# Performance work log

Hardware: AMD Instinct MI355X
Metric: run time of the kernel (lower is better)

## Reference

```python
import jax, jax.numpy as jnp
import numpy as np

VTHR = 1.0


def setup_inputs() -> dict:
    key = jax.random.key(0)
    k1, k2, k3 = jax.random.split(key, 3)
    B, T, IN, OUT = 256, 8, 4096, 4096
    x = jax.random.normal(k1, (B * T, IN), dtype=jnp.float32)
    weight_scaled = jax.random.normal(k2, (OUT, IN), dtype=jnp.float32) * 0.02
    bias_scaled = jax.random.normal(k3, (OUT,), dtype=jnp.float32) * 0.02
    return {"x": x, "weight_scaled": weight_scaled, "bias_scaled": bias_scaled, "timesteps": T}


def _spike_linear(x, weight_scaled, bias_scaled, timesteps):
    # F.linear: [B*T, IN] @ [OUT, IN]^T + [OUT]
    out = jnp.dot(x, weight_scaled.T) + bias_scaled  # [B*T, OUT]
    OUT = out.shape[-1]
    out_s = out.reshape(-1, timesteps, OUT)  # [B, T, OUT]
    out_t = jnp.transpose(out_s, (1, 0, 2))  # [T, B, OUT] for scan

    def step(memb, o_t):
        memb = memb + VTHR * o_t
        spike = (memb > VTHR).astype(out.dtype)
        memb = memb * (1.0 - spike)  # reset_mode == 'zero'
        return memb, spike

    memb0 = jnp.zeros(out_t.shape[1:], dtype=out.dtype)
    _, spikes = jax.lax.scan(step, memb0, out_t)  # [T, B, OUT]
    # torch.cat(spikes, 0): t-major concat -> [T*B, OUT]
    return spikes.reshape(-1, OUT)


def reference(x, weight_scaled, bias_scaled, timesteps):
    return _spike_linear(x, weight_scaled, bias_scaled, timesteps)
```

## Files before the change

### kernel.cpp

```cpp
#include <hip/hip_runtime.h>


typedef float v2f __attribute__((ext_vector_type(2)));

#define PK_LO(a, x, wv)                                                       \
    asm("v_pk_fma_f32 %0, %1, %2, %0 op_sel:[0,0,0] op_sel_hi:[0,1,1]"        \
        : "+v"(a) : "v"(x), "v"(wv))
#define PK_HI(a, x, wv)                                                       \
    asm("v_pk_fma_f32 %0, %1, %2, %0 op_sel:[1,0,0] op_sel_hi:[1,1,1]"        \
        : "+v"(a) : "v"(x), "v"(wv))

constexpr int TSTEPS = 8;
constexpr int BK     = 16;
constexpr int TILE_M = 64;
constexpr int TILE_NP= 256;
constexpr int TILE_N = 128;
constexpr int KC     = 384;

__global__ __launch_bounds__(256, 2)
void spike_panel_gemm(const float* __restrict__ x,
                      const float* __restrict__ w,
                      float* __restrict__ panels,
                      float* __restrict__ out,
                      int slice0, int NW,
                      int B, int IN, int OUT, int npanels)
{
    __shared__ float xs[BK][TILE_M + 4];
    __shared__ float wsh[BK][TILE_NP + 8];

    const int tid  = threadIdx.x;
    const int lane = tid & 63;
    const int wv   = tid >> 6;
    const int rg   = lane >> 3;
    const int cg   = lane & 7;
    const int cbase = wv * 64 + cg * 8;

    const int m0 = blockIdx.y * TILE_M;
    const int n0 = slice0 + blockIdx.x * TILE_NP;
    const int p  = blockIdx.z;
    const int ks = p * KC;
    const int ke = (ks + KC < IN) ? (ks + KC) : IN;

    v2f acc[TSTEPS][4];
    #pragma unroll
    for (int t = 0; t < TSTEPS; ++t)
        #pragma unroll
        for (int q = 0; q < 4; ++q) acc[t][q] = (v2f){0.f, 0.f};

    const int sr = tid >> 2;
    const int sk = (tid & 3) * 4;

    const float* xrow  = x + (size_t)(m0 + sr) * IN + sk;
    const float* wrow0 = w + (size_t)(n0 +       sr) * IN + sk;
    const float* wrow1 = w + (size_t)(n0 +  64 + sr) * IN + sk;
    const float* wrow2 = w + (size_t)(n0 + 128 + sr) * IN + sk;
    const float* wrow3 = w + (size_t)(n0 + 192 + sr) * IN + sk;

    for (int kk = ks; kk < ke; kk += BK) {
        const float4 xv  = *(const float4*)(xrow  + kk);
        const float4 wv0 = *(const float4*)(wrow0 + kk);
        const float4 wv1 = *(const float4*)(wrow1 + kk);
        const float4 wv2 = *(const float4*)(wrow2 + kk);
        const float4 wv3 = *(const float4*)(wrow3 + kk);
        __syncthreads();
        xs[sk+0][sr] = xv.x;  xs[sk+1][sr] = xv.y;
        xs[sk+2][sr] = xv.z;  xs[sk+3][sr] = xv.w;
        wsh[sk+0][sr]     = wv0.x; wsh[sk+1][sr]     = wv0.y;
        wsh[sk+2][sr]     = wv0.z; wsh[sk+3][sr]     = wv0.w;
        wsh[sk+0][sr+64]  = wv1.x; wsh[sk+1][sr+64]  = wv1.y;
        wsh[sk+2][sr+64]  = wv1.z; wsh[sk+3][sr+64]  = wv1.w;
        wsh[sk+0][sr+128] = wv2.x; wsh[sk+1][sr+128] = wv2.y;
        wsh[sk+2][sr+128] = wv2.z; wsh[sk+3][sr+128] = wv2.w;
        wsh[sk+0][sr+192] = wv3.x; wsh[sk+1][sr+192] = wv3.y;
        wsh[sk+2][sr+192] = wv3.z; wsh[sk+3][sr+192] = wv3.w;
        __syncthreads();

        #pragma unroll
        for (int k = 0; k < BK; ++k) {
            v2f xp[4], wva[4];
            *(float4*)&xp[0]  = *(const float4*)&xs[k][rg*8];
            *(float4*)&xp[2]  = *(const float4*)&xs[k][rg*8 + 4];
            *(float4*)&wva[0] = *(const float4*)&wsh[k][cbase];
            *(float4*)&wva[2] = *(const float4*)&wsh[k][cbase + 4];
            #pragma unroll
            for (int tp = 0; tp < 4; ++tp) {
                #pragma unroll
                for (int q = 0; q < 4; ++q) {
                    PK_LO(acc[2*tp  ][q], xp[tp], wva[q]);
                    PK_HI(acc[2*tp+1][q], xp[tp], wva[q]);
                }
            }
        }
    }

    const int bg = blockIdx.y * 8 + rg;
    const int cs = blockIdx.x * TILE_NP + cbase;
    if (p < npanels - 1) {
        float* pb = panels + ((size_t)p * B * TSTEPS) * NW;
        #pragma unroll
        for (int t = 0; t < TSTEPS; ++t) {
            const int m = bg * TSTEPS + t;
            float4 lo, hi;
            *(v2f*)&lo.x = acc[t][0]; *(v2f*)&lo.z = acc[t][1];
            *(v2f*)&hi.x = acc[t][2]; *(v2f*)&hi.z = acc[t][3];
            *(float4*)(pb + (size_t)m * NW + cs)     = lo;
            *(float4*)(pb + (size_t)m * NW + cs + 4) = hi;
        }
    } else {
        const int o0 = n0 + cbase;
        #pragma unroll
        for (int t = 0; t < TSTEPS; ++t) {
            float4 lo, hi;
            *(v2f*)&lo.x = acc[t][0]; *(v2f*)&lo.z = acc[t][1];
            *(v2f*)&hi.x = acc[t][2]; *(v2f*)&hi.z = acc[t][3];
            float* op = out + ((size_t)t * B + bg) * OUT + o0;
            *(float4*)op       = lo;
            *(float4*)(op + 4) = hi;
        }
    }
}

__global__ __launch_bounds__(256)
void spike_fold_scan(const float* __restrict__ panels,
                     const float* __restrict__ bias,
                     float* __restrict__ out,
                     int slice0, int NW,
                     int B, int OUT, int npanels)
{
    const int b = blockIdx.y;
    const size_t psz = (size_t)B * TSTEPS * NW;
    const int nc4 = NW / 4;

    for (int c4 = blockIdx.x * 256 + threadIdx.x; c4 < nc4;
         c4 += gridDim.x * 256) {
        const int cs   = c4 * 4;
        const int gcol = slice0 + cs;

        float4 v[TSTEPS];
        #pragma unroll
        for (int t = 0; t < TSTEPS; ++t)
            v[t] = *(const float4*)(panels + (size_t)(b*TSTEPS + t) * NW + cs);
        for (int p = 1; p < npanels - 1; ++p) {
            const float* pb = panels + (size_t)p * psz;
            #pragma unroll
            for (int t = 0; t < TSTEPS; ++t) {
                const float4 u = *(const float4*)(pb + (size_t)(b*TSTEPS + t) * NW + cs);
                v[t].x += u.x; v[t].y += u.y; v[t].z += u.z; v[t].w += u.w;
            }
        }
        #pragma unroll
        for (int t = 0; t < TSTEPS; ++t) {
            const float4 u = *(const float4*)(out + ((size_t)t * B + b) * OUT + gcol);
            v[t].x += u.x; v[t].y += u.y; v[t].z += u.z; v[t].w += u.w;
        }

        const float4 bb = *(const float4*)(bias + gcol);
        float memb[4] = {0.f, 0.f, 0.f, 0.f};
        #pragma unroll
        for (int t = 0; t < TSTEPS; ++t) {
            float pre[4] = {v[t].x + bb.x, v[t].y + bb.y,
                            v[t].z + bb.z, v[t].w + bb.w};
            float4 sp;
            float* spp = (float*)&sp;
            #pragma unroll
            for (int c = 0; c < 4; ++c) {
                memb[c] += pre[c];
                float s = (memb[c] > 1.0f) ? 1.0f : 0.0f;
                memb[c] *= (1.0f - s);
                spp[c] = s;
            }
            *(float4*)(out + ((size_t)t * B + b) * OUT + gcol) = sp;
        }
    }
}

__global__ __launch_bounds__(256, 4)
void spike_linear_f32seq(const float* __restrict__ x,
                         const float* __restrict__ w,
                         const float* __restrict__ bias,
                         float* __restrict__ out,
                         int B, int IN, int OUT)
{
    __shared__ float xs[BK][TILE_M + 4];
    __shared__ float ws[BK][TILE_N + 4];

    const int tid = threadIdx.x;
    const int tx  = tid & 31;
    const int ty  = tid >> 5;

    const int m0 = blockIdx.y * TILE_M;
    const int n0 = blockIdx.x * TILE_N;

    float acc_tot[TSTEPS][4];
    float acc_blk[TSTEPS][4];
    #pragma unroll
    for (int t = 0; t < TSTEPS; ++t)
        #pragma unroll
        for (int c = 0; c < 4; ++c) { acc_tot[t][c] = 0.f; acc_blk[t][c] = 0.f; }

    const int sr = tid >> 2;
    const int sk = (tid & 3) * 4;

    const float* xrow  = x + (size_t)(m0 + sr) * IN + sk;
    const float* wrow0 = w + (size_t)(n0 + sr) * IN + sk;
    const float* wrow1 = w + (size_t)(n0 + 64 + sr) * IN + sk;

    for (int kk = 0; kk < IN; kk += BK) {
        if (kk > 0 && (kk % KC) == 0) {
            #pragma unroll
            for (int t = 0; t < TSTEPS; ++t)
                #pragma unroll
                for (int c = 0; c < 4; ++c) {
                    acc_tot[t][c] += acc_blk[t][c];
                    acc_blk[t][c] = 0.f;
                }
        }
        const float4 xv  = *(const float4*)(xrow  + kk);
        const float4 wv0 = *(const float4*)(wrow0 + kk);
        const float4 wv1 = *(const float4*)(wrow1 + kk);
        __syncthreads();
        xs[sk+0][sr] = xv.x;  xs[sk+1][sr] = xv.y;
        xs[sk+2][sr] = xv.z;  xs[sk+3][sr] = xv.w;
        ws[sk+0][sr]    = wv0.x; ws[sk+1][sr]    = wv0.y;
        ws[sk+2][sr]    = wv0.z; ws[sk+3][sr]    = wv0.w;
        ws[sk+0][sr+64] = wv1.x; ws[sk+1][sr+64] = wv1.y;
        ws[sk+2][sr+64] = wv1.z; ws[sk+3][sr+64] = wv1.w;
        __syncthreads();

        #pragma unroll
        for (int k = 0; k < BK; ++k) {
            float xr[TSTEPS];
            *(float4*)&xr[0] = *(const float4*)&xs[k][ty*8];
            *(float4*)&xr[4] = *(const float4*)&xs[k][ty*8 + 4];
            float wr[4];
            *(float4*)&wr[0] = *(const float4*)&ws[k][tx*4];
            #pragma unroll
            for (int t = 0; t < TSTEPS; ++t)
                #pragma unroll
                for (int c = 0; c < 4; ++c)
                    acc_blk[t][c] = fmaf(xr[t], wr[c], acc_blk[t][c]);
        }
    }
    #pragma unroll
    for (int t = 0; t < TSTEPS; ++t)
        #pragma unroll
        for (int c = 0; c < 4; ++c)
            acc_tot[t][c] += acc_blk[t][c];

    const int bg = blockIdx.y * 8 + ty;
    const int o0 = n0 + tx * 4;
    const float4 bv = *(const float4*)(bias + o0);
    const float bb[4] = {bv.x, bv.y, bv.z, bv.w};
    float memb[4] = {0.f, 0.f, 0.f, 0.f};
    #pragma unroll
    for (int t = 0; t < TSTEPS; ++t) {
        float4 sp;
        float* spp = (float*)&sp;
        #pragma unroll
        for (int c = 0; c < 4; ++c) {
            float pre = acc_tot[t][c] + bb[c];
            memb[c] += pre;
            float s = (memb[c] > 1.0f) ? 1.0f : 0.0f;
            memb[c] *= (1.0f - s);
            spp[c] = s;
        }
        *(float4*)(out + ((size_t)t * B + bg) * OUT + o0) = sp;
    }
}

extern "C" void kernel_launch(void* const* d_in, const int* in_sizes, int n_in,
                              void* d_out, int out_size, void* d_ws, size_t ws_size,
                              hipStream_t stream)
{
    const float* x    = (const float*)d_in[0];
    const float* w    = (const float*)d_in[1];
    const float* bias = (const float*)d_in[2];
    float* out = (float*)d_out;

    const int OUT = in_sizes[2];
    const int IN  = in_sizes[1] / OUT;
    const int BT  = in_sizes[0] / IN;
    const int B   = BT / TSTEPS;

    const int npanels = (IN + KC - 1) / KC;

    int NW = 0;
    for (int cand = 4096; cand >= 256; cand >>= 1) {
        if ((OUT % cand) == 0 &&
            (size_t)(npanels - 1) * BT * cand * sizeof(float) <= ws_size) {
            NW = cand;
            break;
        }
    }

    if (NW >= 256 && npanels >= 2) {
        float* panels = (float*)d_ws;
        const int nslices = OUT / NW;
        for (int s = 0; s < nslices; ++s) {
            const int slice0 = s * NW;
            dim3 g1(NW / TILE_NP, BT / TILE_M, npanels);
            spike_panel_gemm<<<g1, 256, 0, stream>>>(x, w, panels, out,
                                                     slice0, NW, B, IN, OUT,
                                                     npanels);
            int gx = NW / 1024; if (gx < 1) gx = 1;
            dim3 g2(gx, B);
            spike_fold_scan<<<g2, 256, 0, stream>>>(panels, bias, out,
                                                    slice0, NW, B, OUT,
                                                    npanels);
        }
    } else {
        dim3 grid(OUT / TILE_N, BT / TILE_M);
        spike_linear_f32seq<<<grid, 256, 0, stream>>>(x, w, bias, out, B, IN, OUT);
    }
}
```

Before: 827.3 us.

## Prefetch next K-tile into registers and split column groups to cut LDS conflicts

The GEMM main loop now issues the global loads for the next BK slice right after the LDS stores, so their latency overlaps the FMA work on the current slice (register double-buffering). Each lane's eight output columns are also split into two groups of four spaced 32 apart, with the shared-memory padding reduced accordingly, to change the LDS read pattern and reduce bank conflicts. Output stores follow the new column mapping. Keeping the prefetched tile in registers raises register pressure under launch_bounds(256,2), and K must be a multiple of BK.

```diff
diff --git a/kernel.cpp b/kernel.cpp
--- a/kernel.cpp
+++ b/kernel.cpp
@@ -16,6 +16,7 @@
 constexpr int TILE_NP= 256;
 constexpr int TILE_N = 128;
 constexpr int KC     = 384;
+constexpr int WS_PAD = 4;
 
 __global__ __launch_bounds__(256, 2)
 void spike_panel_gemm(const float* __restrict__ x,
@@ -26,14 +27,14 @@
                       int B, int IN, int OUT, int npanels)
 {
     __shared__ float xs[BK][TILE_M + 4];
-    __shared__ float wsh[BK][TILE_NP + 8];
+    __shared__ float wsh[BK][TILE_NP + WS_PAD];
 
     const int tid  = threadIdx.x;
     const int lane = tid & 63;
     const int wv   = tid >> 6;
     const int rg   = lane >> 3;
     const int cg   = lane & 7;
-    const int cbase = wv * 64 + cg * 8;
+    const int clo  = wv * 64 + cg * 4;
 
     const int m0 = blockIdx.y * TILE_M;
     const int n0 = slice0 + blockIdx.x * TILE_NP;
@@ -56,12 +57,15 @@
     const float* wrow2 = w + (size_t)(n0 + 128 + sr) * IN + sk;
     const float* wrow3 = w + (size_t)(n0 + 192 + sr) * IN + sk;
 
-    for (int kk = ks; kk < ke; kk += BK) {
-        const float4 xv  = *(const float4*)(xrow  + kk);
-        const float4 wv0 = *(const float4*)(wrow0 + kk);
-        const float4 wv1 = *(const float4*)(wrow1 + kk);
-        const float4 wv2 = *(const float4*)(wrow2 + kk);
-        const float4 wv3 = *(const float4*)(wrow3 + kk);
+    const int nsteps = (ke - ks) / BK;
+
+    float4 xv  = *(const float4*)(xrow  + ks);
+    float4 wv0 = *(const float4*)(wrow0 + ks);
+    float4 wv1 = *(const float4*)(wrow1 + ks);
+    float4 wv2 = *(const float4*)(wrow2 + ks);
+    float4 wv3 = *(const float4*)(wrow3 + ks);
+
+    for (int s = 0; s < nsteps; ++s) {
         __syncthreads();
         xs[sk+0][sr] = xv.x;  xs[sk+1][sr] = xv.y;
         xs[sk+2][sr] = xv.z;  xs[sk+3][sr] = xv.w;
@@ -75,13 +79,22 @@
         wsh[sk+2][sr+192] = wv3.z; wsh[sk+3][sr+192] = wv3.w;
         __syncthreads();
 
+        if (s + 1 < nsteps) {
+            const int ko = ks + (s + 1) * BK;
+            xv  = *(const float4*)(xrow  + ko);
+            wv0 = *(const float4*)(wrow0 + ko);
+            wv1 = *(const float4*)(wrow1 + ko);
+            wv2 = *(const float4*)(wrow2 + ko);
+            wv3 = *(const float4*)(wrow3 + ko);
+        }
+
         #pragma unroll
         for (int k = 0; k < BK; ++k) {
             v2f xp[4], wva[4];
             *(float4*)&xp[0]  = *(const float4*)&xs[k][rg*8];
             *(float4*)&xp[2]  = *(const float4*)&xs[k][rg*8 + 4];
-            *(float4*)&wva[0] = *(const float4*)&wsh[k][cbase];
-            *(float4*)&wva[2] = *(const float4*)&wsh[k][cbase + 4];
+            *(float4*)&wva[0] = *(const float4*)&wsh[k][clo];
+            *(float4*)&wva[2] = *(const float4*)&wsh[k][clo + 32];
             #pragma unroll
             for (int tp = 0; tp < 4; ++tp) {
                 #pragma unroll
@@ -94,7 +107,7 @@
     }
 
     const int bg = blockIdx.y * 8 + rg;
-    const int cs = blockIdx.x * TILE_NP + cbase;
+    const int cs = blockIdx.x * TILE_NP + clo;
     if (p < npanels - 1) {
         float* pb = panels + ((size_t)p * B * TSTEPS) * NW;
         #pragma unroll
@@ -103,19 +116,19 @@
             float4 lo, hi;
             *(v2f*)&lo.x = acc[t][0]; *(v2f*)&lo.z = acc[t][1];
             *(v2f*)&hi.x = acc[t][2]; *(v2f*)&hi.z = acc[t][3];
-            *(float4*)(pb + (size_t)m * NW + cs)     = lo;
-            *(float4*)(pb + (size_t)m * NW + cs + 4) = hi;
+            *(float4*)(pb + (size_t)m * NW + cs)      = lo;
+            *(float4*)(pb + (size_t)m * NW + cs + 32) = hi;
         }
     } else {
-        const int o0 = n0 + cbase;
+        const int o0 = n0 + clo;
         #pragma unroll
         for (int t = 0; t < TSTEPS; ++t) {
             float4 lo, hi;
             *(v2f*)&lo.x = acc[t][0]; *(v2f*)&lo.z = acc[t][1];
             *(v2f*)&hi.x = acc[t][2]; *(v2f*)&hi.z = acc[t][3];
             float* op = out + ((size_t)t * B + bg) * OUT + o0;
-            *(float4*)op       = lo;
-            *(float4*)(op + 4) = hi;
+            *(float4*)op        = lo;
+            *(float4*)(op + 32) = hi;
         }
     }
 }
```

New measurement: 800.7 us (median of 2 runs). 3.2% less time.
